# Kernel tuning notes

Hardware: AMD Instinct MI355X
Metric: run time of the kernel (lower is better)

The kernel has to match this reference:

```python
import jax, jax.numpy as jnp
import numpy as np

B, T, C = 4, 2048, 1024
NUM_HEADS, HEAD_DIM = 16, 64
INNER = NUM_HEADS * HEAD_DIM
OUT_DIM = 1024


def setup_inputs() -> dict:
    key = jax.random.key(0)
    kx, kk, kq, kv, kp = jax.random.split(key, 5)
    return {
        "x": jax.random.normal(kx, (B, T, C), dtype=jnp.float32),
        "W_k": jax.random.normal(kk, (INNER, C), dtype=jnp.float32),
        "W_q": jax.random.normal(kq, (INNER, C), dtype=jnp.float32),
        "W_v": jax.random.normal(kv, (INNER, C), dtype=jnp.float32),
        "W_p": jax.random.normal(kp, (OUT_DIM, INNER), dtype=jnp.float32),
    }


def reference(x, W_k, W_q, W_v, W_p):
    b, t, c = x.shape
    h, d = NUM_HEADS, HEAD_DIM
    scale_in = c ** (-0.5)
    # project and split heads: [B, H, T, D]
    def proj(W):
        y = jnp.einsum('btc,ic->bti', x, W) * scale_in
        return y.reshape(b, t, h, d).transpose(0, 2, 1, 3)
    k = proj(W_k)
    q = proj(W_q)
    v = proj(W_v)
    scores = jnp.einsum('bhqd,bhkd->bhqk', q, k) * (d ** (-0.5))
    weight = jax.nn.softmax(scores, axis=-1)
    out = jnp.einsum('bhqk,bhkd->bhqd', weight, v)  # [B,H,T,D]
    out = out.transpose(0, 2, 1, 3).reshape(b, t, h * d)
    out = jnp.einsum('bti,oi->bto', out, W_p) * (W_p.shape[-1] ** (-0.5))
    return out
```

## Files before the change

### kernel.cpp

```cpp
#include <hip/hip_runtime.h>
#include <math.h>

typedef __attribute__((ext_vector_type(8))) short bh8;
typedef __attribute__((ext_vector_type(4))) float f32x4;
typedef __attribute__((ext_vector_type(2))) unsigned u32x2;

namespace {
constexpr int Bn = 4, Tn = 2048, Cn = 1024, Hn = 16, Dn = 64, INNERn = 1024, OUTn = 1024;
constexpr int Mn = Bn * Tn;
}

__device__ __forceinline__ void glds16(const void* g, void* l) {
    __builtin_amdgcn_global_load_lds(
        (const __attribute__((address_space(1))) void*)g,
        (__attribute__((address_space(3))) void*)l, 16, 0, 0);
}

__device__ __forceinline__ void barrier_vm0() {
    __builtin_amdgcn_s_waitcnt(0x0070);
    __builtin_amdgcn_s_barrier();
}

__device__ __forceinline__ ushort f2bf(float f) {
    union { float f; unsigned u; } v; v.f = f;
    unsigned r = v.u + 0x7fffu + ((v.u >> 16) & 1u);
    return (ushort)(r >> 16);
}
__device__ __forceinline__ unsigned pack_rne(float a, float b) {
    return (unsigned)f2bf(a) | ((unsigned)f2bf(b) << 16);
}
__device__ __forceinline__ unsigned pack_trunc(float a, float b) {
    return __builtin_amdgcn_perm(__float_as_uint(a), __float_as_uint(b), 0x03020706u);
}

__global__ __launch_bounds__(256)
void cvt_all(const float* __restrict__ x,  const float* __restrict__ Wk,
             const float* __restrict__ Wq, const float* __restrict__ Wv,
             const float* __restrict__ Wp,
             ushort* __restrict__ xb,  ushort* __restrict__ wkb,
             ushort* __restrict__ wqb, ushort* __restrict__ wvb,
             ushort* __restrict__ wpb)
{
    const int bid = blockIdx.x;
    const float* s; ushort* d; float sc; int i;
    if (bid < 8192) {
        s = x; d = xb; sc = 0.03125f;
        i = bid * 256 + threadIdx.x;
    } else {
        const int seg = (bid - 8192) >> 10;
        i = ((bid - 8192) & 1023) * 256 + threadIdx.x;
        s  = (seg == 0) ? Wk : (seg == 1) ? Wq : (seg == 2) ? Wv : Wp;
        d  = (seg == 0) ? wkb : (seg == 1) ? wqb : (seg == 2) ? wvb : wpb;
        sc = (seg == 3) ? 0.03125f : 1.0f;
    }
    float4 f = ((const float4*)s)[i];
    ushort4 o;
    o.x = f2bf(f.x * sc); o.y = f2bf(f.y * sc);
    o.z = f2bf(f.z * sc); o.w = f2bf(f.w * sc);
    ((ushort4*)d)[i] = o;
}

__global__ __launch_bounds__(256)
void gemm_qkv(const ushort* __restrict__ A, const ushort* __restrict__ Wq,
              const ushort* __restrict__ Wk, const ushort* __restrict__ Wv,
              ushort* __restrict__ Oq, ushort* __restrict__ Ok,
              ushort* __restrict__ Ovt, float qscale)
{
    __shared__ char SM[32768];
    char* As0 = SM;          char* As1 = SM + 8192;
    char* Bs0 = SM + 16384;  char* Bs1 = SM + 24576;
    const int tid = threadIdx.x;
    const int w = tid >> 6, lane = tid & 63, quad = lane >> 4, l = lane & 15;
    const int sel = blockIdx.x >> 3;
    const ushort* Bw = (sel == 0) ? Wq : (sel == 1) ? Wk : Wv;
    const int n0 = (blockIdx.x & 7) * 128, m0 = blockIdx.y * 128;
    const int wm = w >> 1, wn = w & 1;

    auto stage = [&](char* Ad, char* Bd, int k0) {
#pragma unroll
        for (int rr = 0; rr < 2; ++rr) {
            const int rho = w * 2 + rr;
            const int row = rho * 16 + (lane >> 2);
            const int kq  = (lane & 3) * 8;
            glds16(A  + (size_t)(m0 + row) * Cn + k0 + kq, Ad + rho * 1024 + lane * 16);
            glds16(Bw + (size_t)(n0 + row) * Cn + k0 + kq, Bd + rho * 1024 + lane * 16);
        }
    };

    f32x4 acc[4][4];
#pragma unroll
    for (int i = 0; i < 4; ++i)
#pragma unroll
        for (int j = 0; j < 4; ++j) acc[i][j] = (f32x4){0.f, 0.f, 0.f, 0.f};

    stage(As0, Bs0, 0);
    barrier_vm0();
#pragma unroll 2
    for (int it = 0; it < 32; ++it) {
        const int cur = it & 1;
        if (it < 31) stage(cur ? As0 : As1, cur ? Bs0 : Bs1, (it + 1) * 32);
        const char* Ac = cur ? As1 : As0; const char* Bc = cur ? Bs1 : Bs0;
        bh8 af[4], bf[4];
#pragma unroll
        for (int mf = 0; mf < 4; ++mf)
            af[mf] = *(const bh8*)(Ac + (wm * 64 + mf * 16 + l) * 64 + quad * 16);
#pragma unroll
        for (int nf = 0; nf < 4; ++nf)
            bf[nf] = *(const bh8*)(Bc + (wn * 64 + nf * 16 + l) * 64 + quad * 16);
#pragma unroll
        for (int mf = 0; mf < 4; ++mf)
#pragma unroll
            for (int nf = 0; nf < 4; ++nf)
                acc[mf][nf] = __builtin_amdgcn_mfma_f32_16x16x32_bf16(af[mf], bf[nf], acc[mf][nf], 0, 0, 0);
        barrier_vm0();
    }

    if (sel < 2) {
        ushort* dU = (sel == 0) ? Oq : Ok;
        const float scale = (sel == 0) ? qscale : 1.0f;
#pragma unroll
        for (int mf = 0; mf < 4; ++mf)
#pragma unroll
            for (int nf = 0; nf < 4; ++nf) {
                const int mb = m0 + wm * 64 + mf * 16 + quad * 4;
                const int n  = n0 + wn * 64 + nf * 16 + l;
                const int h = n >> 6, dd = n & 63;
#pragma unroll
                for (int reg = 0; reg < 4; ++reg) {
                    const int m = mb + reg;
                    const int b = m >> 11, t = m & (Tn - 1);
                    dU[((size_t)(b * Hn + h) * Tn + t) * Dn + dd] = f2bf(acc[mf][nf][reg] * scale);
                }
            }
    } else {
#pragma unroll
        for (int mf = 0; mf < 4; ++mf)
#pragma unroll
            for (int nf = 0; nf < 4; ++nf) {
                const int mb = wm * 64 + mf * 16 + quad * 4;
                const int n  = wn * 64 + nf * 16 + l;
                uint2 p;
                p.x = pack_rne(acc[mf][nf][0], acc[mf][nf][1]);
                p.y = pack_rne(acc[mf][nf][2], acc[mf][nf][3]);
                const int c = mb >> 3;
                *(uint2*)(SM + n * 256 + ((c ^ (n & 15)) & 15) * 16 + (mb & 7) * 2) = p;
            }
        __syncthreads();
        const int bb = m0 >> 11, t0 = m0 & (Tn - 1);
#pragma unroll
        for (int it2 = 0; it2 < 8; ++it2) {
            const int n = it2 * 16 + w * 4 + quad;
            const int ng = n0 + n;
            const int h = ng >> 6, dd = ng & 63;
            int4 vsm = *(const int4*)(SM + n * 256 + ((l ^ (n & 15)) & 15) * 16);
            *(int4*)(Ovt + ((size_t)(bb * Hn + h) * Dn + dd) * Tn + t0 + l * 8) = vsm;
        }
    }
}

__global__ __launch_bounds__(256)
void gemm_po(const ushort* __restrict__ A, const ushort* __restrict__ Bw,
             float* __restrict__ Cout)
{
    __shared__ char As[2][8192];
    __shared__ char Bs[2][8192];
    const int tid = threadIdx.x;
    const int w = tid >> 6, lane = tid & 63, quad = lane >> 4, l = lane & 15;
    const int n0 = blockIdx.x * 128, m0 = blockIdx.y * 128;
    const int wm = w >> 1, wn = w & 1;

    auto stage = [&](int bsel, int k0) {
#pragma unroll
        for (int rr = 0; rr < 2; ++rr) {
            const int rho = w * 2 + rr;
            const int row = rho * 16 + (lane >> 2);
            const int kq  = (lane & 3) * 8;
            glds16(A  + (size_t)(m0 + row) * Cn + k0 + kq, As[bsel] + rho * 1024 + lane * 16);
            glds16(Bw + (size_t)(n0 + row) * Cn + k0 + kq, Bs[bsel] + rho * 1024 + lane * 16);
        }
    };

    f32x4 acc[4][4];
#pragma unroll
    for (int i = 0; i < 4; ++i)
#pragma unroll
        for (int j = 0; j < 4; ++j) acc[i][j] = (f32x4){0.f, 0.f, 0.f, 0.f};

    stage(0, 0);
    barrier_vm0();
#pragma unroll 2
    for (int it = 0; it < 32; ++it) {
        const int cur = it & 1;
        if (it < 31) stage(cur ^ 1, (it + 1) * 32);
        const char* Ac = As[cur]; const char* Bc = Bs[cur];
        bh8 af[4], bf[4];
#pragma unroll
        for (int mf = 0; mf < 4; ++mf)
            af[mf] = *(const bh8*)(Ac + (wm * 64 + mf * 16 + l) * 64 + quad * 16);
#pragma unroll
        for (int nf = 0; nf < 4; ++nf)
            bf[nf] = *(const bh8*)(Bc + (wn * 64 + nf * 16 + l) * 64 + quad * 16);
#pragma unroll
        for (int mf = 0; mf < 4; ++mf)
#pragma unroll
            for (int nf = 0; nf < 4; ++nf)
                acc[mf][nf] = __builtin_amdgcn_mfma_f32_16x16x32_bf16(af[mf], bf[nf], acc[mf][nf], 0, 0, 0);
        barrier_vm0();
    }

#pragma unroll
    for (int mf = 0; mf < 4; ++mf)
#pragma unroll
        for (int nf = 0; nf < 4; ++nf) {
            const int mb = m0 + wm * 64 + mf * 16 + quad * 4;
            const int n  = n0 + wn * 64 + nf * 16 + l;
#pragma unroll
            for (int reg = 0; reg < 4; ++reg)
                Cout[(size_t)(mb + reg) * OUTn + n] = acc[mf][nf][reg];
        }
}

__global__ __launch_bounds__(256, 4)
void attn_mfma(const ushort* __restrict__ Qg, const ushort* __restrict__ Kg,
               const ushort* __restrict__ Vtg, ushort* __restrict__ Og)
{
    __shared__ char KT[2][8192];
    __shared__ char VT[2][8192];

    const int tid = threadIdx.x;
    const int w = tid >> 6, lane = tid & 63, quad = lane >> 4, l = lane & 15;
    const int q0 = blockIdx.x * 128;
    const int bh = blockIdx.y, b = bh >> 4, h = bh & 15;
    const ushort* Qp = Qg  + (size_t)bh * Tn * Dn;
    const ushort* Kp = Kg  + (size_t)bh * Tn * Dn;
    const ushort* Vp = Vtg + (size_t)bh * Dn * Tn;

    auto stageK = [&](char* buf, int kt) {
#pragma unroll
        for (int rr = 0; rr < 2; ++rr) {
            const int rho = w * 2 + rr;
            const int r8  = lane >> 3;
            const int r   = rho * 8 + r8;
            const int dc  = (lane & 7) ^ r8;
            glds16(Kp + (size_t)(kt * 64 + r) * Dn + dc * 8, buf + rho * 1024 + lane * 16);
        }
    };
    auto stageV = [&](char* buf, int kt) {
#pragma unroll
        for (int rr = 0; rr < 2; ++rr) {
            const int rho = w * 2 + rr;
            const int d = rho * 8 + (lane >> 3);
            const int csrc = (lane & 7) ^ ((lane >> 3) & 7);
            glds16(Vp + (size_t)d * Tn + kt * 64 + csrc * 8, buf + rho * 1024 + lane * 16);
        }
    };

    bh8 qf[2][2];
#pragma unroll
    for (int nt = 0; nt < 2; ++nt)
#pragma unroll
        for (int ks = 0; ks < 2; ++ks)
            qf[nt][ks] = *(const bh8*)(Qp + (size_t)(q0 + w * 32 + nt * 16 + l) * Dn + ks * 32 + quad * 8);

    bh8 ones;
#pragma unroll
    for (int i = 0; i < 8; ++i) ones[i] = (short)0x3F80;

    f32x4 oacc[2][4], lacc[2];
#pragma unroll
    for (int nt = 0; nt < 2; ++nt) {
        lacc[nt] = (f32x4){0.f, 0.f, 0.f, 0.f};
#pragma unroll
        for (int dt = 0; dt < 4; ++dt) oacc[nt][dt] = (f32x4){0.f, 0.f, 0.f, 0.f};
    }

    const f32x4 zero = (f32x4){0.f, 0.f, 0.f, 0.f};

    stageK(KT[0], 0);
    stageV(VT[0], 0);
    barrier_vm0();

#pragma unroll 2
    for (int kt = 0; kt < Tn / 64; ++kt) {
        const int cur = kt & 1;
        if (kt < Tn / 64 - 1) {
            stageK(KT[cur ^ 1], kt + 1);
            stageV(VT[cur ^ 1], kt + 1);
        }
        const char* Kc = KT[cur];
        const char* Vc = VT[cur];

#pragma unroll
        for (int hh = 0; hh < 2; ++hh) {
            bh8 kf[2][2];
#pragma unroll
            for (int k8l = 0; k8l < 2; ++k8l) {
                const int row = (hh * 2 + k8l) * 16 + l;
#pragma unroll
                for (int ks = 0; ks < 2; ++ks)
                    kf[k8l][ks] = *(const bh8*)(Kc + row * 128 + (((ks * 4 + quad) ^ (l & 7)) * 16));
            }

            f32x4 st[2][2];
#pragma unroll
            for (int nt = 0; nt < 2; ++nt)
#pragma unroll
                for (int k8l = 0; k8l < 2; ++k8l) {
                    st[nt][k8l] = __builtin_amdgcn_mfma_f32_16x16x32_bf16(kf[k8l][0], qf[nt][0], zero, 0, 0, 0);
                    st[nt][k8l] = __builtin_amdgcn_mfma_f32_16x16x32_bf16(kf[k8l][1], qf[nt][1], st[nt][k8l], 0, 0, 0);
                }

            bh8 pf[2];
#pragma unroll
            for (int nt = 0; nt < 2; ++nt) {
                const unsigned a0 = pack_trunc(__builtin_amdgcn_exp2f(st[nt][0][0]),
                                               __builtin_amdgcn_exp2f(st[nt][0][1]));
                const unsigned a1 = pack_trunc(__builtin_amdgcn_exp2f(st[nt][0][2]),
                                               __builtin_amdgcn_exp2f(st[nt][0][3]));
                const unsigned b0 = pack_trunc(__builtin_amdgcn_exp2f(st[nt][1][0]),
                                               __builtin_amdgcn_exp2f(st[nt][1][1]));
                const unsigned b1 = pack_trunc(__builtin_amdgcn_exp2f(st[nt][1][2]),
                                               __builtin_amdgcn_exp2f(st[nt][1][3]));
                const u32x2 p = __builtin_amdgcn_permlane32_swap(a0, b0, false, false);
                const u32x2 q = __builtin_amdgcn_permlane16_swap(p.x, p.y, false, false);
                const u32x2 r = __builtin_amdgcn_permlane32_swap(a1, b1, false, false);
                const u32x2 s = __builtin_amdgcn_permlane16_swap(r.x, r.y, false, false);
                union { unsigned u[4]; bh8 v; } pu;
                pu.u[0] = q.x; pu.u[1] = s.x; pu.u[2] = q.y; pu.u[3] = s.y;
                pf[nt] = pu.v;
            }

#pragma unroll
            for (int nt = 0; nt < 2; ++nt)
                lacc[nt] = __builtin_amdgcn_mfma_f32_16x16x32_bf16(ones, pf[nt], lacc[nt], 0, 0, 0);
#pragma unroll
            for (int dt = 0; dt < 4; ++dt) {
                bh8 vf = *(const bh8*)(Vc + (dt * 16 + l) * 128 + (((hh * 4 + quad) ^ (l & 7)) * 16));
#pragma unroll
                for (int nt = 0; nt < 2; ++nt)
                    oacc[nt][dt] = __builtin_amdgcn_mfma_f32_16x16x32_bf16(vf, pf[nt], oacc[nt][dt], 0, 0, 0);
            }
        }
        barrier_vm0();
    }

#pragma unroll
    for (int nt = 0; nt < 2; ++nt) {
        const float inv = 1.0f / lacc[nt][0];
        const int t = q0 + w * 32 + nt * 16 + l;
#pragma unroll
        for (int dt = 0; dt < 4; ++dt) {
            uint2 p;
            p.x = pack_rne(oacc[nt][dt][0] * inv, oacc[nt][dt][1] * inv);
            p.y = pack_rne(oacc[nt][dt][2] * inv, oacc[nt][dt][3] * inv);
            *(uint2*)(Og + ((size_t)(b * Tn + t)) * INNERn + h * 64 + dt * 16 + quad * 4) = p;
        }
    }
}

extern "C" void kernel_launch(void* const* d_in, const int* in_sizes, int n_in,
                              void* d_out, int out_size, void* d_ws, size_t ws_size,
                              hipStream_t stream)
{
    const float* x  = (const float*)d_in[0];
    const float* Wk = (const float*)d_in[1];
    const float* Wq = (const float*)d_in[2];
    const float* Wv = (const float*)d_in[3];
    const float* Wp = (const float*)d_in[4];
    float* out = (float*)d_out;

    ushort* xb  = (ushort*)d_ws;
    ushort* wkb = xb  + (size_t)Mn * Cn;
    ushort* wqb = wkb + (size_t)INNERn * Cn;
    ushort* wvb = wqb + (size_t)INNERn * Cn;
    ushort* wpb = wvb + (size_t)INNERn * Cn;
    ushort* qw  = wpb + (size_t)OUTn * INNERn;
    ushort* kw  = qw  + (size_t)Mn * INNERn;
    ushort* vtw = kw  + (size_t)Mn * INNERn;
    ushort* aow = vtw + (size_t)Mn * INNERn;

    const dim3 blk(256);
    cvt_all<<<dim3(8192 + 4096), blk, 0, stream>>>(x, Wk, Wq, Wv, Wp,
                                                   xb, wkb, wqb, wvb, wpb);

    gemm_qkv<<<dim3(3 * 8, Mn / 128), blk, 0, stream>>>(xb, wqb, wkb, wvb,
                                                        qw, kw, vtw, 0.125f * 1.44269504f);

    attn_mfma<<<dim3(Tn / 128, Bn * Hn), blk, 0, stream>>>(qw, kw, vtw, aow);

    gemm_po<<<dim3(OUTn / 128, Mn / 128), blk, 0, stream>>>(aow, wpb, out);
}
```

Before: 270.1 us.

## Remap blocks to XCDs, halve attention query tile, add MFMA priority hints

All three GEMM and attention launches become 1D grids. Block ids are remapped so consecutive tiles sharing operands land on the same XCD, which is meant to improve L2 reuse of weights, K and V. The attention kernel now handles 64 queries per block (16 per wave) instead of 128, doubling the grid and cutting register use. s_setprio brackets the MFMA sections. The smaller query tile doubles K/V staging traffic per query, so each loaded K/V tile is reused less.

```diff
diff --git a/kernel.cpp b/kernel.cpp
--- a/kernel.cpp
+++ b/kernel.cpp
@@ -71,9 +71,13 @@
     char* Bs0 = SM + 16384;  char* Bs1 = SM + 24576;
     const int tid = threadIdx.x;
     const int w = tid >> 6, lane = tid & 63, quad = lane >> 4, l = lane & 15;
-    const int sel = blockIdx.x >> 3;
+    const int lid = blockIdx.x;
+    const int xcd = lid & 7, j = lid >> 3;
+    const int ytile = xcd * 8 + j / 24;
+    const int xx = j % 24;
+    const int sel = xx >> 3;
     const ushort* Bw = (sel == 0) ? Wq : (sel == 1) ? Wk : Wv;
-    const int n0 = (blockIdx.x & 7) * 128, m0 = blockIdx.y * 128;
+    const int n0 = (xx & 7) * 128, m0 = ytile * 128;
     const int wm = w >> 1, wn = w & 1;
 
     auto stage = [&](char* Ad, char* Bd, int k0) {
@@ -91,7 +95,7 @@
 #pragma unroll
     for (int i = 0; i < 4; ++i)
 #pragma unroll
-        for (int j = 0; j < 4; ++j) acc[i][j] = (f32x4){0.f, 0.f, 0.f, 0.f};
+        for (int j2 = 0; j2 < 4; ++j2) acc[i][j2] = (f32x4){0.f, 0.f, 0.f, 0.f};
 
     stage(As0, Bs0, 0);
     barrier_vm0();
@@ -166,7 +170,9 @@
     __shared__ char Bs[2][8192];
     const int tid = threadIdx.x;
     const int w = tid >> 6, lane = tid & 63, quad = lane >> 4, l = lane & 15;
-    const int n0 = blockIdx.x * 128, m0 = blockIdx.y * 128;
+    const int lid = blockIdx.x;
+    const int xcd = lid & 7, j = lid >> 3;
+    const int n0 = (j & 7) * 128, m0 = (xcd * 8 + (j >> 3)) * 128;
     const int wm = w >> 1, wn = w & 1;
 
     auto stage = [&](int bsel, int k0) {
@@ -184,7 +190,7 @@
 #pragma unroll
     for (int i = 0; i < 4; ++i)
 #pragma unroll
-        for (int j = 0; j < 4; ++j) acc[i][j] = (f32x4){0.f, 0.f, 0.f, 0.f};
+        for (int j2 = 0; j2 < 4; ++j2) acc[i][j2] = (f32x4){0.f, 0.f, 0.f, 0.f};
 
     stage(0, 0);
     barrier_vm0();
@@ -229,8 +235,11 @@
 
     const int tid = threadIdx.x;
     const int w = tid >> 6, lane = tid & 63, quad = lane >> 4, l = lane & 15;
-    const int q0 = blockIdx.x * 128;
-    const int bh = blockIdx.y, b = bh >> 4, h = bh & 15;
+    const int lid = blockIdx.x;
+    const int xcd = lid & 7, j = lid >> 3;
+    const int bh = (xcd << 3) | (j >> 5);
+    const int q0 = (j & 31) * 64;
+    const int b = bh >> 4, h = bh & 15;
     const ushort* Qp = Qg  + (size_t)bh * Tn * Dn;
     const ushort* Kp = Kg  + (size_t)bh * Tn * Dn;
     const ushort* Vp = Vtg + (size_t)bh * Dn * Tn;
@@ -255,24 +264,19 @@
         }
     };
 
-    bh8 qf[2][2];
-#pragma unroll
-    for (int nt = 0; nt < 2; ++nt)
-#pragma unroll
-        for (int ks = 0; ks < 2; ++ks)
-            qf[nt][ks] = *(const bh8*)(Qp + (size_t)(q0 + w * 32 + nt * 16 + l) * Dn + ks * 32 + quad * 8);
+    bh8 qf[2];
+#pragma unroll
+    for (int ks = 0; ks < 2; ++ks)
+        qf[ks] = *(const bh8*)(Qp + (size_t)(q0 + w * 16 + l) * Dn + ks * 32 + quad * 8);
 
     bh8 ones;
 #pragma unroll
     for (int i = 0; i < 8; ++i) ones[i] = (short)0x3F80;
 
-    f32x4 oacc[2][4], lacc[2];
-#pragma unroll
-    for (int nt = 0; nt < 2; ++nt) {
-        lacc[nt] = (f32x4){0.f, 0.f, 0.f, 0.f};
-#pragma unroll
-        for (int dt = 0; dt < 4; ++dt) oacc[nt][dt] = (f32x4){0.f, 0.f, 0.f, 0.f};
-    }
+    f32x4 oacc[4], lacc;
+    lacc = (f32x4){0.f, 0.f, 0.f, 0.f};
+#pragma unroll
+    for (int dt = 0; dt < 4; ++dt) oacc[dt] = (f32x4){0.f, 0.f, 0.f, 0.f};
 
     const f32x4 zero = (f32x4){0.f, 0.f, 0.f, 0.f};
 
@@ -301,58 +305,53 @@
                     kf[k8l][ks] = *(const bh8*)(Kc + row * 128 + (((ks * 4 + quad) ^ (l & 7)) * 16));
             }
 
-            f32x4 st[2][2];
-#pragma unroll
-            for (int nt = 0; nt < 2; ++nt)
-#pragma unroll
-                for (int k8l = 0; k8l < 2; ++k8l) {
-                    st[nt][k8l] = __builtin_amdgcn_mfma_f32_16x16x32_bf16(kf[k8l][0], qf[nt][0], zero, 0, 0, 0);
-                    st[nt][k8l] = __builtin_amdgcn_mfma_f32_16x16x32_bf16(kf[k8l][1], qf[nt][1], st[nt][k8l], 0, 0, 0);
-                }
-
-            bh8 pf[2];
-#pragma unroll
-            for (int nt = 0; nt < 2; ++nt) {
-                const unsigned a0 = pack_trunc(__builtin_amdgcn_exp2f(st[nt][0][0]),
-                                               __builtin_amdgcn_exp2f(st[nt][0][1]));
-                const unsigned a1 = pack_trunc(__builtin_amdgcn_exp2f(st[nt][0][2]),
-                                               __builtin_amdgcn_exp2f(st[nt][0][3]));
-                const unsigned b0 = pack_trunc(__builtin_amdgcn_exp2f(st[nt][1][0]),
-                                               __builtin_amdgcn_exp2f(st[nt][1][1]));
-                const unsigned b1 = pack_trunc(__builtin_amdgcn_exp2f(st[nt][1][2]),
-                                               __builtin_amdgcn_exp2f(st[nt][1][3]));
-                const u32x2 p = __builtin_amdgcn_permlane32_swap(a0, b0, false, false);
-                const u32x2 q = __builtin_amdgcn_permlane16_swap(p.x, p.y, false, false);
-                const u32x2 r = __builtin_amdgcn_permlane32_swap(a1, b1, false, false);
-                const u32x2 s = __builtin_amdgcn_permlane16_swap(r.x, r.y, false, false);
-                union { unsigned u[4]; bh8 v; } pu;
-                pu.u[0] = q.x; pu.u[1] = s.x; pu.u[2] = q.y; pu.u[3] = s.y;
-                pf[nt] = pu.v;
+            f32x4 st[2];
+            __builtin_amdgcn_s_setprio(1);
+#pragma unroll
+            for (int k8l = 0; k8l < 2; ++k8l) {
+                st[k8l] = __builtin_amdgcn_mfma_f32_16x16x32_bf16(kf[k8l][0], qf[0], zero, 0, 0, 0);
+                st[k8l] = __builtin_amdgcn_mfma_f32_16x16x32_bf16(kf[k8l][1], qf[1], st[k8l], 0, 0, 0);
             }
-
-#pragma unroll
-            for (int nt = 0; nt < 2; ++nt)
-                lacc[nt] = __builtin_amdgcn_mfma_f32_16x16x32_bf16(ones, pf[nt], lacc[nt], 0, 0, 0);
-#pragma unroll
-            for (int dt = 0; dt < 4; ++dt) {
-                bh8 vf = *(const bh8*)(Vc + (dt * 16 + l) * 128 + (((hh * 4 + quad) ^ (l & 7)) * 16));
-#pragma unroll
-                for (int nt = 0; nt < 2; ++nt)
-                    oacc[nt][dt] = __builtin_amdgcn_mfma_f32_16x16x32_bf16(vf, pf[nt], oacc[nt][dt], 0, 0, 0);
-            }
+            __builtin_amdgcn_s_setprio(0);
+
+            const unsigned a0 = pack_trunc(__builtin_amdgcn_exp2f(st[0][0]),
+                                           __builtin_amdgcn_exp2f(st[0][1]));
+            const unsigned a1 = pack_trunc(__builtin_amdgcn_exp2f(st[0][2]),
+                                           __builtin_amdgcn_exp2f(st[0][3]));
+            const unsigned b0 = pack_trunc(__builtin_amdgcn_exp2f(st[1][0]),
+                                           __builtin_amdgcn_exp2f(st[1][1]));
+            const unsigned b1 = pack_trunc(__builtin_amdgcn_exp2f(st[1][2]),
+                                           __builtin_amdgcn_exp2f(st[1][3]));
+            const u32x2 p = __builtin_amdgcn_permlane32_swap(a0, b0, false, false);
+            const u32x2 q = __builtin_amdgcn_permlane16_swap(p.x, p.y, false, false);
+            const u32x2 r = __builtin_amdgcn_permlane32_swap(a1, b1, false, false);
+            const u32x2 s = __builtin_amdgcn_permlane16_swap(r.x, r.y, false, false);
+            union { unsigned u[4]; bh8 v; } pu;
+            pu.u[0] = q.x; pu.u[1] = s.x; pu.u[2] = q.y; pu.u[3] = s.y;
+            const bh8 pf = pu.v;
+
+            bh8 vf[4];
+#pragma unroll
+            for (int dt = 0; dt < 4; ++dt)
+                vf[dt] = *(const bh8*)(Vc + (dt * 16 + l) * 128 + (((hh * 4 + quad) ^ (l & 7)) * 16));
+            __builtin_amdgcn_s_setprio(1);
+            lacc = __builtin_amdgcn_mfma_f32_16x16x32_bf16(ones, pf, lacc, 0, 0, 0);
+#pragma unroll
+            for (int dt = 0; dt < 4; ++dt)
+                oacc[dt] = __builtin_amdgcn_mfma_f32_16x16x32_bf16(vf[dt], pf, oacc[dt], 0, 0, 0);
+            __builtin_amdgcn_s_setprio(0);
         }
         barrier_vm0();
     }
 
-#pragma unroll
-    for (int nt = 0; nt < 2; ++nt) {
-        const float inv = 1.0f / lacc[nt][0];
-        const int t = q0 + w * 32 + nt * 16 + l;
+    {
+        const float inv = 1.0f / lacc[0];
+        const int t = q0 + w * 16 + l;
 #pragma unroll
         for (int dt = 0; dt < 4; ++dt) {
             uint2 p;
-            p.x = pack_rne(oacc[nt][dt][0] * inv, oacc[nt][dt][1] * inv);
-            p.y = pack_rne(oacc[nt][dt][2] * inv, oacc[nt][dt][3] * inv);
+            p.x = pack_rne(oacc[dt][0] * inv, oacc[dt][1] * inv);
+            p.y = pack_rne(oacc[dt][2] * inv, oacc[dt][3] * inv);
             *(uint2*)(Og + ((size_t)(b * Tn + t)) * INNERn + h * 64 + dt * 16 + quad * 4) = p;
         }
     }
@@ -383,10 +382,10 @@
     cvt_all<<<dim3(8192 + 4096), blk, 0, stream>>>(x, Wk, Wq, Wv, Wp,
                                                    xb, wkb, wqb, wvb, wpb);
 
-    gemm_qkv<<<dim3(3 * 8, Mn / 128), blk, 0, stream>>>(xb, wqb, wkb, wvb,
-                                                        qw, kw, vtw, 0.125f * 1.44269504f);
-
-    attn_mfma<<<dim3(Tn / 128, Bn * Hn), blk, 0, stream>>>(qw, kw, vtw, aow);
-
-    gemm_po<<<dim3(OUTn / 128, Mn / 128), blk, 0, stream>>>(aow, wpb, out);
-}
+    gemm_qkv<<<dim3(1536), blk, 0, stream>>>(xb, wqb, wkb, wvb,
+                                             qw, kw, vtw, 0.125f * 1.44269504f);
+
+    attn_mfma<<<dim3(2048), blk, 0, stream>>>(qw, kw, vtw, aow);
+
+    gemm_po<<<dim3(512), blk, 0, stream>>>(aow, wpb, out);
+}
```

Result: no change. 272.3 us (+0.8%).

## Remap block IDs for XCD-local L2 reuse and add MFMA priority hints in attention

Applied to the files above, without the earlier changes.

All three main kernels now launch on a 1D grid and remap the block index so that blocks scheduled on the same XCD (lid & 7) work on neighbouring M tiles or the same batch-head. The goal is shared L2 reuse of A rows and K/V tiles within each XCD. The attention kernel also hoists the four V fragment LDS loads ahead of the PV MFMA loop and wraps the MFMA sections in s_setprio, so other waves can do exp/permute work while these run. The index math adds a little integer overhead, and the speedup relies on the hardware dispatching blocks round-robin across XCDs.

```diff
diff --git a/kernel.cpp b/kernel.cpp
--- a/kernel.cpp
+++ b/kernel.cpp
@@ -71,9 +71,13 @@
     char* Bs0 = SM + 16384;  char* Bs1 = SM + 24576;
     const int tid = threadIdx.x;
     const int w = tid >> 6, lane = tid & 63, quad = lane >> 4, l = lane & 15;
-    const int sel = blockIdx.x >> 3;
+    const int lid = blockIdx.x;
+    const int xcd = lid & 7, j = lid >> 3;
+    const int ytile = xcd * 8 + j / 24;
+    const int xx = j % 24;
+    const int sel = xx >> 3;
     const ushort* Bw = (sel == 0) ? Wq : (sel == 1) ? Wk : Wv;
-    const int n0 = (blockIdx.x & 7) * 128, m0 = blockIdx.y * 128;
+    const int n0 = (xx & 7) * 128, m0 = ytile * 128;
     const int wm = w >> 1, wn = w & 1;
 
     auto stage = [&](char* Ad, char* Bd, int k0) {
@@ -91,7 +95,7 @@
 #pragma unroll
     for (int i = 0; i < 4; ++i)
 #pragma unroll
-        for (int j = 0; j < 4; ++j) acc[i][j] = (f32x4){0.f, 0.f, 0.f, 0.f};
+        for (int j2 = 0; j2 < 4; ++j2) acc[i][j2] = (f32x4){0.f, 0.f, 0.f, 0.f};
 
     stage(As0, Bs0, 0);
     barrier_vm0();
@@ -166,7 +170,9 @@
     __shared__ char Bs[2][8192];
     const int tid = threadIdx.x;
     const int w = tid >> 6, lane = tid & 63, quad = lane >> 4, l = lane & 15;
-    const int n0 = blockIdx.x * 128, m0 = blockIdx.y * 128;
+    const int lid = blockIdx.x;
+    const int xcd = lid & 7, j = lid >> 3;
+    const int n0 = (j & 7) * 128, m0 = (xcd * 8 + (j >> 3)) * 128;
     const int wm = w >> 1, wn = w & 1;
 
     auto stage = [&](int bsel, int k0) {
@@ -184,7 +190,7 @@
 #pragma unroll
     for (int i = 0; i < 4; ++i)
 #pragma unroll
-        for (int j = 0; j < 4; ++j) acc[i][j] = (f32x4){0.f, 0.f, 0.f, 0.f};
+        for (int j2 = 0; j2 < 4; ++j2) acc[i][j2] = (f32x4){0.f, 0.f, 0.f, 0.f};
 
     stage(0, 0);
     barrier_vm0();
@@ -229,8 +235,11 @@
 
     const int tid = threadIdx.x;
     const int w = tid >> 6, lane = tid & 63, quad = lane >> 4, l = lane & 15;
-    const int q0 = blockIdx.x * 128;
-    const int bh = blockIdx.y, b = bh >> 4, h = bh & 15;
+    const int lid = blockIdx.x;
+    const int xcd = lid & 7, j = lid >> 3;
+    const int bh = (xcd << 3) | (j >> 4);
+    const int q0 = (j & 15) * 128;
+    const int b = bh >> 4, h = bh & 15;
     const ushort* Qp = Qg  + (size_t)bh * Tn * Dn;
     const ushort* Kp = Kg  + (size_t)bh * Tn * Dn;
     const ushort* Vp = Vtg + (size_t)bh * Dn * Tn;
@@ -302,6 +311,7 @@
             }
 
             f32x4 st[2][2];
+            __builtin_amdgcn_s_setprio(1);
 #pragma unroll
             for (int nt = 0; nt < 2; ++nt)
 #pragma unroll
@@ -309,6 +319,7 @@
                     st[nt][k8l] = __builtin_amdgcn_mfma_f32_16x16x32_bf16(kf[k8l][0], qf[nt][0], zero, 0, 0, 0);
                     st[nt][k8l] = __builtin_amdgcn_mfma_f32_16x16x32_bf16(kf[k8l][1], qf[nt][1], st[nt][k8l], 0, 0, 0);
                 }
+            __builtin_amdgcn_s_setprio(0);
 
             bh8 pf[2];
 #pragma unroll
@@ -330,16 +341,20 @@
                 pf[nt] = pu.v;
             }
 
+            bh8 vf[4];
+#pragma unroll
+            for (int dt = 0; dt < 4; ++dt)
+                vf[dt] = *(const bh8*)(Vc + (dt * 16 + l) * 128 + (((hh * 4 + quad) ^ (l & 7)) * 16));
+            __builtin_amdgcn_s_setprio(1);
 #pragma unroll
             for (int nt = 0; nt < 2; ++nt)
                 lacc[nt] = __builtin_amdgcn_mfma_f32_16x16x32_bf16(ones, pf[nt], lacc[nt], 0, 0, 0);
 #pragma unroll
-            for (int dt = 0; dt < 4; ++dt) {
-                bh8 vf = *(const bh8*)(Vc + (dt * 16 + l) * 128 + (((hh * 4 + quad) ^ (l & 7)) * 16));
+            for (int dt = 0; dt < 4; ++dt)
 #pragma unroll
                 for (int nt = 0; nt < 2; ++nt)
-                    oacc[nt][dt] = __builtin_amdgcn_mfma_f32_16x16x32_bf16(vf, pf[nt], oacc[nt][dt], 0, 0, 0);
-            }
+                    oacc[nt][dt] = __builtin_amdgcn_mfma_f32_16x16x32_bf16(vf[dt], pf[nt], oacc[nt][dt], 0, 0, 0);
+            __builtin_amdgcn_s_setprio(0);
         }
         barrier_vm0();
     }
@@ -383,10 +398,10 @@
     cvt_all<<<dim3(8192 + 4096), blk, 0, stream>>>(x, Wk, Wq, Wv, Wp,
                                                    xb, wkb, wqb, wvb, wpb);
 
-    gemm_qkv<<<dim3(3 * 8, Mn / 128), blk, 0, stream>>>(xb, wqb, wkb, wvb,
-                                                        qw, kw, vtw, 0.125f * 1.44269504f);
-
-    attn_mfma<<<dim3(Tn / 128, Bn * Hn), blk, 0, stream>>>(qw, kw, vtw, aow);
-
-    gemm_po<<<dim3(OUTn / 128, Mn / 128), blk, 0, stream>>>(aow, wpb, out);
-}
+    gemm_qkv<<<dim3(1536), blk, 0, stream>>>(xb, wqb, wkb, wvb,
+                                             qw, kw, vtw, 0.125f * 1.44269504f);
+
+    attn_mfma<<<dim3(1024), blk, 0, stream>>>(qw, kw, vtw, aow);
+
+    gemm_po<<<dim3(512), blk, 0, stream>>>(aow, wpb, out);
+}
```

After: 256.7 us. 1.05x faster.
